# Performance work log

Hardware: AMD Instinct MI355X
Metric: run time of the kernel (lower is better)

## Reference

```python
import jax, jax.numpy as jnp
import numpy as np

B, S, H = 2, 1024, 4096
NQ, NKV, D = 32, 8, 128
I = 11008
EPS = 1e-5


def _rope_tables(seq_len, head_dim, base=10000.0):
    inv_freq = 1.0 / (base ** (np.arange(0, head_dim, 2, dtype=np.float32) / head_dim))
    t = np.arange(seq_len, dtype=np.float32)
    freqs = np.outer(t, inv_freq)                      # [S, D/2]
    emb = np.concatenate([freqs, freqs], axis=-1)      # [S, D]
    return jnp.asarray(np.cos(emb)), jnp.asarray(np.sin(emb))


def setup_inputs() -> dict:
    key = jax.random.key(0)
    ks = jax.random.split(key, 9)
    sc = 0.02
    cos, sin = _rope_tables(S, D)
    return {
        "x": jax.random.normal(ks[0], (B, S, H), jnp.float32),
        "cos": cos,
        "sin": sin,
        "attn_norm_w": jnp.ones((H,), jnp.float32),
        "ffn_norm_w": jnp.ones((H,), jnp.float32),
        "wq": jax.random.normal(ks[1], (H, NQ * D), jnp.float32) * sc,
        "wk": jax.random.normal(ks[2], (H, NKV * D), jnp.float32) * sc,
        "wv": jax.random.normal(ks[3], (H, NKV * D), jnp.float32) * sc,
        "wo": jax.random.normal(ks[4], (NQ * D, H), jnp.float32) * sc,
        "w_gate": jax.random.normal(ks[5], (H, I), jnp.float32) * sc,
        "w_up": jax.random.normal(ks[6], (H, I), jnp.float32) * sc,
        "w_down": jax.random.normal(ks[7], (I, H), jnp.float32) * sc,
    }


def _rmsnorm(x, w, eps=EPS):
    var = jnp.mean(jnp.square(x), axis=-1, keepdims=True)
    return x * jax.lax.rsqrt(var + eps) * w


def _rotate_half(x):
    x1, x2 = jnp.split(x, 2, axis=-1)
    return jnp.concatenate([-x2, x1], axis=-1)


def _apply_rope(q, k, cos, sin):
    # q: [B,S,NQ,D], k: [B,S,NKV,D]; cos/sin: [S,D] -> broadcast [1,S,1,D]
    c = cos[None, :, None, :]
    s = sin[None, :, None, :]
    return q * c + _rotate_half(q) * s, k * c + _rotate_half(k) * s


def reference(x, cos, sin, attn_norm_w, ffn_norm_w, wq, wk, wv, wo, w_gate, w_up, w_down):
    # ---- attention block (pre-norm, context/prefill path, causal) ----
    h_in = _rmsnorm(x, attn_norm_w)
    q = (h_in @ wq).reshape(B, S, NQ, D)
    k = (h_in @ wk).reshape(B, S, NKV, D)
    v = (h_in @ wv).reshape(B, S, NKV, D)
    q, k = _apply_rope(q, k, cos, sin)

    n_rep = NQ // NKV
    k = jnp.repeat(k, n_rep, axis=2)  # [B,S,NQ,D]
    v = jnp.repeat(v, n_rep, axis=2)

    scale = 1.0 / jnp.sqrt(jnp.float32(D))
    scores = jnp.einsum("bqhd,bkhd->bhqk", q, k) * scale  # [B,NQ,S,S]
    causal = jnp.tril(jnp.ones((S, S), bool))
    scores = jnp.where(causal[None, None], scores, -jnp.inf)
    probs = jax.nn.softmax(scores, axis=-1)
    attn = jnp.einsum("bhqk,bkhd->bqhd", probs, v).reshape(B, S, NQ * D)
    h = x + attn @ wo

    # ---- MLP block (pre-norm SwiGLU) ----
    m_in = _rmsnorm(h, ffn_norm_w)
    mlp = (jax.nn.silu(m_in @ w_gate) * (m_in @ w_up)) @ w_down
    return h + mlp
```

## Files before the change

### kernel.cpp

```cpp
#include <hip/hip_runtime.h>
#include <cstdint>
#include <cstddef>


typedef __bf16 bf16;
typedef __attribute__((ext_vector_type(8))) __bf16 bf16x8;
typedef __attribute__((ext_vector_type(4))) float f32x4;

#define GLDS16(gptr, lptr)                                                    \
  __builtin_amdgcn_global_load_lds(                                           \
      (const __attribute__((address_space(1))) void*)(gptr),                  \
      (__attribute__((address_space(3))) void*)(lptr), 16, 0, 0)

#define S_LEN 1024
#define H_DIM 4096
#define NQ_H 32
#define NKV_H 8
#define HD 128
#define I_DIM 11008

__global__ __launch_bounds__(256) void wtrans64_kernel(
    const float* __restrict__ src, bf16* __restrict__ dst, int K, int N,
    int tile_stride, int base) {
  const int tid = threadIdx.x;
  const int n0 = blockIdx.x * 64, k0 = blockIdx.y * 64;
  __shared__ float t[64][65];
  const int r = tid >> 4, c4 = (tid & 15) * 4;
#pragma unroll
  for (int j = 0; j < 4; j++) {
    const float4 v =
        *(const float4*)&src[(size_t)(k0 + r + j * 16) * N + n0 + c4];
    t[r + j * 16][c4 + 0] = v.x;
    t[r + j * 16][c4 + 1] = v.y;
    t[r + j * 16][c4 + 2] = v.z;
    t[r + j * 16][c4 + 3] = v.w;
  }
  __syncthreads();
  const int n = tid >> 2, kq = (tid & 3) * 16;
  bf16x8 o0, o1;
#pragma unroll
  for (int i = 0; i < 8; i++) {
    o0[i] = (bf16)t[kq + i][n];
    o1[i] = (bf16)t[kq + 8 + i][n];
  }
  const int ng = n0 + n;
  const size_t orow = (size_t)(ng >> 7) * tile_stride + (ng & 127) + base;
  *(bf16x8*)&dst[orow * K + k0 + kq] = o0;
  *(bf16x8*)&dst[orow * K + k0 + kq + 8] = o1;
}

__global__ __launch_bounds__(256) void rmsnorm_kernel(
    const float* __restrict__ x, const float* __restrict__ w,
    bf16* __restrict__ out) {
  const int row = blockIdx.x;
  const float4* xr = (const float4*)(x + (size_t)row * H_DIM);
  float4 v[4];
  float s = 0.f;
#pragma unroll
  for (int i = 0; i < 4; i++) {
    v[i] = xr[threadIdx.x + i * 256];
    s += v[i].x * v[i].x + v[i].y * v[i].y + v[i].z * v[i].z + v[i].w * v[i].w;
  }
#pragma unroll
  for (int m = 1; m < 64; m <<= 1) s += __shfl_xor(s, m);
  __shared__ float red[4];
  if ((threadIdx.x & 63) == 0) red[threadIdx.x >> 6] = s;
  __syncthreads();
  s = red[0] + red[1] + red[2] + red[3];
  const float r = rsqrtf(s * (1.f / H_DIM) + 1e-5f);
  bf16* o = out + (size_t)row * H_DIM;
  const float4* wr = (const float4*)w;
#pragma unroll
  for (int i = 0; i < 4; i++) {
    float4 wv = wr[threadIdx.x + i * 256];
    int idx = (threadIdx.x + i * 256) * 4;
    o[idx + 0] = (bf16)(v[i].x * r * wv.x);
    o[idx + 1] = (bf16)(v[i].y * r * wv.y);
    o[idx + 2] = (bf16)(v[i].z * r * wv.z);
    o[idx + 3] = (bf16)(v[i].w * r * wv.w);
  }
}

template <int BM, int MODE>
__global__ __launch_bounds__(512, 2) void gemm256(
    const bf16* __restrict__ A, const bf16* __restrict__ Bt,
    void* __restrict__ Cout, const float* __restrict__ resid, int N, int K,
    int mshift) {
  constexpr int MREP = BM / 32;
  constexpr int MQ = MREP / 2;
  constexpr int LA = BM / 128;
  constexpr int ABYTES = BM * 128;
  constexpr int BUFB = ABYTES + 32768;
  __shared__ __align__(16) char smem[2 * BUFB];

  const int tid = threadIdx.x;
  const int w = tid >> 6, lane = tid & 63;
  const int lr = lane & 15, quad = lane >> 4;
  const int wm = w & 1, wn = w >> 1;
  const int m0 = (blockIdx.x & ((1 << mshift) - 1)) * BM;
  const int n0 = (blockIdx.x >> mshift) * 256;
  const int NT = K >> 6;

  const int lrow = lane >> 3;
  const int lcbe = ((lane & 7) ^ lrow) << 3;
  const bf16* aS[2][LA];
#pragma unroll
  for (int h = 0; h < 2; h++)
#pragma unroll
    for (int j = 0; j < LA; j++)
      aS[h][j] =
          A + (size_t)(m0 + h * (BM / 2) + j * 64 + w * 8 + lrow) * K + lcbe;
  const bf16* bS[2][2];
#pragma unroll
  for (int h = 0; h < 2; h++)
#pragma unroll
    for (int j = 0; j < 2; j++)
      bS[h][j] =
          Bt + (size_t)(n0 + h * 128 + j * 64 + w * 8 + lrow) * K + lcbe;
  const int sdst = w * 1024;

#pragma unroll
  for (int h = 0; h < 2; h++)
#pragma unroll
    for (int j = 0; j < 2; j++)
      GLDS16(bS[h][j], smem + ABYTES + h * 16384 + j * 8192 + sdst);
#pragma unroll
  for (int h = 0; h < 2; h++)
#pragma unroll
    for (int j = 0; j < LA; j++)
      GLDS16(aS[h][j], smem + h * (BM * 64) + j * 8192 + sdst);
#pragma unroll
  for (int h = 0; h < 2; h++)
#pragma unroll
    for (int j = 0; j < 2; j++)
      GLDS16(bS[h][j] + 64, smem + BUFB + ABYTES + h * 16384 + j * 8192 + sdst);
  asm volatile("s_waitcnt vmcnt(4)" ::: "memory");
  __builtin_amdgcn_s_barrier();

  const int swz = (lr & 7) << 4;
  const int abase = (wm * (BM / 2) + lr) * 128;
  const int bbase = ABYTES + (wn * 64 + lr) * 128;
  const int pcb0 = (quad * 16) ^ swz;

  f32x4 acc[MREP][4] = {};
  bf16x8 af[MQ][2], bfr[2][2][2];

  for (int t = 0; t < NT; ++t) {
    char* cb_ = smem + (t & 1) * BUFB;
    char* nb_ = smem + ((t & 1) ^ 1) * BUFB;

#pragma unroll
    for (int i4 = 0; i4 < MQ; i4++)
#pragma unroll
      for (int kk = 0; kk < 2; kk++)
        af[i4][kk] = *(const bf16x8*)(cb_ + abase + i4 * (16 * 128) +
                                      (pcb0 ^ (kk * 64)));
#pragma unroll
    for (int j2 = 0; j2 < 2; j2++)
#pragma unroll
      for (int kk = 0; kk < 2; kk++)
        bfr[0][j2][kk] = *(const bf16x8*)(cb_ + bbase + j2 * (16 * 128) +
                                          (pcb0 ^ (kk * 64)));
    if (t + 1 < NT) {
#pragma unroll
      for (int j = 0; j < LA; j++)
        GLDS16(aS[0][j] + (size_t)(t + 1) * 64, nb_ + j * 8192 + sdst);
    }
    __builtin_amdgcn_s_barrier();
    asm volatile("s_waitcnt lgkmcnt(0)" ::: "memory");
    __builtin_amdgcn_sched_barrier(0);
    __builtin_amdgcn_s_setprio(1);
#pragma unroll
    for (int i4 = 0; i4 < MQ; i4++)
#pragma unroll
      for (int j2 = 0; j2 < 2; j2++)
#pragma unroll
        for (int kk = 0; kk < 2; kk++)
          acc[i4][j2] = __builtin_amdgcn_mfma_f32_16x16x32_bf16(
              af[i4][kk], bfr[0][j2][kk], acc[i4][j2], 0, 0, 0);
    __builtin_amdgcn_s_setprio(0);
    __builtin_amdgcn_s_barrier();

#pragma unroll
    for (int j2 = 0; j2 < 2; j2++)
#pragma unroll
      for (int kk = 0; kk < 2; kk++)
        bfr[1][j2][kk] =
            *(const bf16x8*)(cb_ + bbase + (32 + j2 * 16) * 128 +
                             (pcb0 ^ (kk * 64)));
    if (t + 1 < NT) {
#pragma unroll
      for (int j = 0; j < LA; j++)
        GLDS16(aS[1][j] + (size_t)(t + 1) * 64,
               nb_ + BM * 64 + j * 8192 + sdst);
    }
    __builtin_amdgcn_s_barrier();
    asm volatile("s_waitcnt lgkmcnt(0)" ::: "memory");
    __builtin_amdgcn_sched_barrier(0);
    __builtin_amdgcn_s_setprio(1);
#pragma unroll
    for (int i4 = 0; i4 < MQ; i4++)
#pragma unroll
      for (int j2 = 0; j2 < 2; j2++)
#pragma unroll
        for (int kk = 0; kk < 2; kk++)
          acc[i4][2 + j2] = __builtin_amdgcn_mfma_f32_16x16x32_bf16(
              af[i4][kk], bfr[1][j2][kk], acc[i4][2 + j2], 0, 0, 0);
    __builtin_amdgcn_s_setprio(0);
    __builtin_amdgcn_s_barrier();

#pragma unroll
    for (int i4 = 0; i4 < MQ; i4++)
#pragma unroll
      for (int kk = 0; kk < 2; kk++)
        af[i4][kk] =
            *(const bf16x8*)(cb_ + abase + ((BM / 4) + i4 * 16) * 128 +
                             (pcb0 ^ (kk * 64)));
    if (t + 2 < NT) {
#pragma unroll
      for (int j = 0; j < 2; j++)
        GLDS16(bS[0][j] + (size_t)(t + 2) * 64,
               cb_ + ABYTES + j * 8192 + sdst);
    }
    __builtin_amdgcn_s_barrier();
    asm volatile("s_waitcnt lgkmcnt(0)" ::: "memory");
    __builtin_amdgcn_sched_barrier(0);
    __builtin_amdgcn_s_setprio(1);
#pragma unroll
    for (int i4 = 0; i4 < MQ; i4++)
#pragma unroll
      for (int j2 = 0; j2 < 2; j2++)
#pragma unroll
        for (int kk = 0; kk < 2; kk++)
          acc[MQ + i4][j2] = __builtin_amdgcn_mfma_f32_16x16x32_bf16(
              af[i4][kk], bfr[0][j2][kk], acc[MQ + i4][j2], 0, 0, 0);
    __builtin_amdgcn_s_setprio(0);
    __builtin_amdgcn_s_barrier();

    if (t + 2 < NT) {
#pragma unroll
      for (int j = 0; j < 2; j++)
        GLDS16(bS[1][j] + (size_t)(t + 2) * 64,
               cb_ + ABYTES + 16384 + j * 8192 + sdst);
    }
    __builtin_amdgcn_s_barrier();
    asm volatile("s_waitcnt lgkmcnt(0)" ::: "memory");
    __builtin_amdgcn_sched_barrier(0);
    __builtin_amdgcn_s_setprio(1);
#pragma unroll
    for (int i4 = 0; i4 < MQ; i4++)
#pragma unroll
      for (int j2 = 0; j2 < 2; j2++)
#pragma unroll
        for (int kk = 0; kk < 2; kk++)
          acc[MQ + i4][2 + j2] = __builtin_amdgcn_mfma_f32_16x16x32_bf16(
              af[i4][kk], bfr[1][j2][kk], acc[MQ + i4][2 + j2], 0, 0, 0);
    __builtin_amdgcn_s_setprio(0);
    if (t + 2 < NT)
      asm volatile("s_waitcnt vmcnt(4)" ::: "memory");
    else
      asm volatile("s_waitcnt vmcnt(0)" ::: "memory");
    __builtin_amdgcn_s_barrier();
  }

#pragma unroll
  for (int ai = 0; ai < MREP; ai++)
#pragma unroll
    for (int bj = 0; bj < 4; bj++)
#pragma unroll
      for (int r = 0; r < 4; r++) {
        const size_t row = m0 + wm * (BM / 2) + ai * 16 + quad * 4 + r;
        const size_t col = n0 + wn * 64 + bj * 16 + lr;
        const float v = acc[ai][bj][r];
        if (MODE == 0)
          ((bf16*)Cout)[row * N + col] = (bf16)v;
        else
          ((float*)Cout)[row * N + col] = v + resid[row * N + col];
      }
}

__global__ __launch_bounds__(256) void rope_kernel(
    const bf16* __restrict__ qkv, const float* __restrict__ cosT,
    const float* __restrict__ sinT, bf16* __restrict__ qb,
    bf16* __restrict__ kb) {
  const int row = blockIdx.x;
  const int s = row & (S_LEN - 1);
  const bf16* base = qkv + (size_t)row * 6144;
  const float scale = 0.08838834764831845f;
  for (int p = threadIdx.x; p < 2560; p += 256) {
    const int hd = p >> 6;
    const int d = p & 63;
    const float c = cosT[s * HD + d], sn = sinT[s * HD + d];
    if (hd < NQ_H) {
      const bf16* qp = base + hd * HD;
      const float x1 = (float)qp[d], x2 = (float)qp[d + 64];
      bf16* o = qb + (size_t)row * H_DIM + hd * HD;
      o[d] = (bf16)((x1 * c - x2 * sn) * scale);
      o[d + 64] = (bf16)((x2 * c + x1 * sn) * scale);
    } else {
      const int kh = hd - NQ_H;
      const bf16* kp = base + H_DIM + kh * HD;
      const float x1 = (float)kp[d], x2 = (float)kp[d + 64];
      bf16* o = kb + (size_t)row * (NKV_H * HD) + kh * HD;
      o[d] = (bf16)(x1 * c - x2 * sn);
      o[d + 64] = (bf16)(x2 * c + x1 * sn);
    }
  }
}

__global__ __launch_bounds__(256) void vtrans_kernel(
    const bf16* __restrict__ qkv, bf16* __restrict__ vt) {
  const int tx = threadIdx.x & 31, ty = threadIdx.x >> 5;
  const int s0 = blockIdx.x * 32, d0 = blockIdx.y * 32;
  const int b = blockIdx.z >> 3, kv = blockIdx.z & 7;
  __shared__ float t[32][33];
#pragma unroll
  for (int j = 0; j < 4; j++) {
    const int s = s0 + ty + j * 8;
    t[ty + j * 8][tx] =
        (float)qkv[(size_t)(b * S_LEN + s) * 6144 + 5120 + kv * HD + d0 + tx];
  }
  __syncthreads();
#pragma unroll
  for (int j = 0; j < 4; j++) {
    const int d = d0 + ty + j * 8;
    vt[((size_t)(b * NKV_H + kv) * HD + d) * S_LEN + s0 + tx] =
        (bf16)t[tx][ty + j * 8];
  }
}

__global__ __launch_bounds__(256) void attn_fwd(
    const bf16* __restrict__ Qb, const bf16* __restrict__ Kb,
    const bf16* __restrict__ Vtb, bf16* __restrict__ Ob) {
  __shared__ __align__(16) bf16 Ks[16 * 512];
  __shared__ __align__(16) bf16 Vs[16 * 512];
  __shared__ __align__(16) bf16 Ps[16 * 512];
  const int tid = threadIdx.x;
  const int wave = tid >> 6, lane = tid & 63;
  const int lr = lane & 15, quad = lane >> 4;
  const int qt = blockIdx.x, h = blockIdx.y, b = blockIdx.z;
  const int kv = h >> 2;
  const int qrow0 = qt * 128 + wave * 32;

  bf16x8 qf[2][4];
#pragma unroll
  for (int mi = 0; mi < 2; mi++)
#pragma unroll
    for (int ks = 0; ks < 4; ks++)
      qf[mi][ks] = *(const bf16x8*)&Qb[(size_t)(b * S_LEN + qrow0 + mi * 16 + lr) *
                                           H_DIM +
                                       h * HD + ks * 32 + quad * 8];

  f32x4 oacc[2][8] = {};
  float m_i[2][4], l_i[2][4];
#pragma unroll
  for (int mi = 0; mi < 2; mi++)
#pragma unroll
    for (int r = 0; r < 4; r++) {
      m_i[mi][r] = -__builtin_inff();
      l_i[mi][r] = 0.f;
    }

  const int nk = 2 * (qt + 1);
  const int maxrow = qrow0 + 31;
  const int srow = lane >> 2;
  const int scol = (lane & 3) * 8;

  for (int kt = 0; kt < nk; kt++) {
    const int k0 = kt * 64;
    __syncthreads();
#pragma unroll
    for (int i = 0; i < 4; i++) {
      const int c = wave * 4 + i;
      {
        const int ks = c >> 2, sc = c & 3;
        const int key = sc * 16 + srow;
        GLDS16(Kb + (size_t)(b * S_LEN + k0 + key) * (NKV_H * HD) + kv * HD +
                   ks * 32 + scol,
               Ks + c * 512);
      }
      {
        const int ks2 = c >> 3, sc2 = c & 7;
        const int d = sc2 * 16 + srow;
        GLDS16(Vtb + ((size_t)(b * NKV_H + kv) * HD + d) * S_LEN + k0 +
                   ks2 * 32 + scol,
               Vs + c * 512);
      }
    }
    __syncthreads();
    const bool active = (k0 <= maxrow);
    float alpha[2][4];
    if (active) {
      f32x4 sacc[2][4];
#pragma unroll
      for (int mi = 0; mi < 2; mi++)
#pragma unroll
        for (int nj = 0; nj < 4; nj++) sacc[mi][nj] = (f32x4){0.f, 0.f, 0.f, 0.f};
#pragma unroll
      for (int ks = 0; ks < 4; ks++) {
        bf16x8 kf[4];
#pragma unroll
        for (int nj = 0; nj < 4; nj++)
          kf[nj] = *(const bf16x8*)&Ks[ks * 2048 + (nj * 16 + lr) * 32 + quad * 8];
#pragma unroll
        for (int mi = 0; mi < 2; mi++)
#pragma unroll
          for (int nj = 0; nj < 4; nj++)
            sacc[mi][nj] = __builtin_amdgcn_mfma_f32_16x16x32_bf16(
                qf[mi][ks], kf[nj], sacc[mi][nj], 0, 0, 0);
      }
#pragma unroll
      for (int mi = 0; mi < 2; mi++) {
#pragma unroll
        for (int r = 0; r < 4; r++) {
          const int row = qrow0 + mi * 16 + quad * 4 + r;
          float best = -__builtin_inff();
#pragma unroll
          for (int nj = 0; nj < 4; nj++) {
            const int col = k0 + nj * 16 + lr;
            if (col > row) sacc[mi][nj][r] = -__builtin_inff();
            best = fmaxf(best, sacc[mi][nj][r]);
          }
#pragma unroll
          for (int m = 1; m < 16; m <<= 1)
            best = fmaxf(best, __shfl_xor(best, m));
          const float mnew = fmaxf(m_i[mi][r], best);
          alpha[mi][r] = __expf(m_i[mi][r] - mnew);
          m_i[mi][r] = mnew;
          float ssum = 0.f;
#pragma unroll
          for (int nj = 0; nj < 4; nj++) {
            const float p = __expf(sacc[mi][nj][r] - mnew);
            sacc[mi][nj][r] = p;
            ssum += p;
          }
#pragma unroll
          for (int m = 1; m < 16; m <<= 1) ssum += __shfl_xor(ssum, m);
          l_i[mi][r] = l_i[mi][r] * alpha[mi][r] + ssum;
        }
      }
#pragma unroll
      for (int mi = 0; mi < 2; mi++)
#pragma unroll
        for (int dj = 0; dj < 8; dj++)
#pragma unroll
          for (int r = 0; r < 4; r++) oacc[mi][dj][r] *= alpha[mi][r];
#pragma unroll
      for (int mi = 0; mi < 2; mi++)
#pragma unroll
        for (int nj = 0; nj < 4; nj++) {
          const int ks2 = nj >> 1;
          const int k32 = (nj & 1) * 16 + lr;
#pragma unroll
          for (int r = 0; r < 4; r++) {
            const int rowl = wave * 32 + mi * 16 + quad * 4 + r;
            Ps[ks2 * 4096 + rowl * 32 + k32] = (bf16)sacc[mi][nj][r];
          }
        }
    }
    __syncthreads();
    if (active) {
#pragma unroll
      for (int ks2 = 0; ks2 < 2; ks2++) {
        bf16x8 pf[2], vf[8];
#pragma unroll
        for (int mi = 0; mi < 2; mi++)
          pf[mi] = *(const bf16x8*)&Ps[ks2 * 4096 +
                                       (wave * 32 + mi * 16 + lr) * 32 + quad * 8];
#pragma unroll
        for (int dj = 0; dj < 8; dj++)
          vf[dj] = *(const bf16x8*)&Vs[ks2 * 4096 + (dj * 16 + lr) * 32 + quad * 8];
#pragma unroll
        for (int mi = 0; mi < 2; mi++)
#pragma unroll
          for (int dj = 0; dj < 8; dj++)
            oacc[mi][dj] = __builtin_amdgcn_mfma_f32_16x16x32_bf16(
                pf[mi], vf[dj], oacc[mi][dj], 0, 0, 0);
      }
    }
  }
#pragma unroll
  for (int mi = 0; mi < 2; mi++)
#pragma unroll
    for (int r = 0; r < 4; r++) {
      const float rinv = 1.f / l_i[mi][r];
      const size_t row = (size_t)b * S_LEN + qrow0 + mi * 16 + quad * 4 + r;
#pragma unroll
      for (int dj = 0; dj < 8; dj++)
        Ob[row * H_DIM + h * HD + dj * 16 + lr] =
            (bf16)(oacc[mi][dj][r] * rinv);
    }
}

__global__ __launch_bounds__(256) void swiglu_kernel(
    const bf16* __restrict__ gu, bf16* __restrict__ act) {
  const int gid = blockIdx.x * 256 + threadIdx.x;
  const int row = gid / 1376;
  const int c8 = (gid % 1376) * 8;
  const size_t gbase = (size_t)row * 22016 + (size_t)(c8 >> 7) * 256 + (c8 & 127);
  bf16x8 g = *(const bf16x8*)&gu[gbase];
  bf16x8 u = *(const bf16x8*)&gu[gbase + 128];
  bf16x8 o;
#pragma unroll
  for (int j = 0; j < 8; j++) {
    const float gf = (float)g[j];
    const float sg = gf / (1.f + __expf(-gf));
    o[j] = (bf16)(sg * (float)u[j]);
  }
  *(bf16x8*)&act[(size_t)row * I_DIM + c8] = o;
}

extern "C" void kernel_launch(void* const* d_in, const int* in_sizes, int n_in,
                              void* d_out, int out_size, void* d_ws,
                              size_t ws_size, hipStream_t stream) {
  const float* x = (const float*)d_in[0];
  const float* cosT = (const float*)d_in[1];
  const float* sinT = (const float*)d_in[2];
  const float* anw = (const float*)d_in[3];
  const float* fnw = (const float*)d_in[4];
  const float* wq = (const float*)d_in[5];
  const float* wk = (const float*)d_in[6];
  const float* wv = (const float*)d_in[7];
  const float* wo = (const float*)d_in[8];
  const float* wg = (const float*)d_in[9];
  const float* wu = (const float*)d_in[10];
  const float* wd = (const float*)d_in[11];

  char* ws = (char*)d_ws;
  size_t off = 0;
  auto alloc = [&](size_t bytes) -> void* {
    void* p = ws + off;
    off += (bytes + 255) & ~(size_t)255;
    return p;
  };
  const size_t M = 2048;
  bf16* WGUt = (bf16*)alloc(22016ULL * 4096 * 2);
  bf16* WDt = (bf16*)alloc(4096ULL * I_DIM * 2);
  char* R1 = (char*)alloc(90177536);
  char* bufY = (char*)alloc(83886080);
  float* H2 = (float*)alloc(M * 4096 * 4);
  bf16* MINb = (bf16*)alloc(M * 4096 * 2);

  bf16* WQKVt = (bf16*)R1;
  bf16* WOt = (bf16*)(R1 + 50331648);
  bf16* GU = (bf16*)R1;
  bf16* HIN = (bf16*)bufY;
  bf16* QKVb = HIN + M * 4096;
  bf16* QB = QKVb + M * 6144;
  bf16* KB = QB + M * 4096;
  bf16* VT = KB + M * 1024;
  bf16* ATTN = VT + M * 1024;
  bf16* ACT = (bf16*)bufY;

  wtrans64_kernel<<<dim3(64, 64), 256, 0, stream>>>(wq, WQKVt, 4096, 4096, 128, 0);
  wtrans64_kernel<<<dim3(16, 64), 256, 0, stream>>>(wk, WQKVt + 4096ULL * 4096, 4096, 1024, 128, 0);
  wtrans64_kernel<<<dim3(16, 64), 256, 0, stream>>>(wv, WQKVt + 5120ULL * 4096, 4096, 1024, 128, 0);
  wtrans64_kernel<<<dim3(64, 64), 256, 0, stream>>>(wo, WOt, 4096, 4096, 128, 0);
  wtrans64_kernel<<<dim3(172, 64), 256, 0, stream>>>(wg, WGUt, 4096, I_DIM, 256, 0);
  wtrans64_kernel<<<dim3(172, 64), 256, 0, stream>>>(wu, WGUt, 4096, I_DIM, 256, 128);
  wtrans64_kernel<<<dim3(64, 172), 256, 0, stream>>>(wd, WDt, I_DIM, 4096, 128, 0);

  rmsnorm_kernel<<<2048, 256, 0, stream>>>(x, anw, HIN);
  gemm256<256, 0><<<8 * 24, 512, 0, stream>>>(HIN, WQKVt, QKVb, nullptr, 6144, 4096, 3);
  rope_kernel<<<2048, 256, 0, stream>>>(QKVb, cosT, sinT, QB, KB);
  vtrans_kernel<<<dim3(32, 4, 16), 256, 0, stream>>>(QKVb, VT);
  attn_fwd<<<dim3(8, 32, 2), 256, 0, stream>>>(QB, KB, VT, ATTN);
  gemm256<128, 2><<<16 * 16, 512, 0, stream>>>(ATTN, WOt, H2, x, 4096, 4096, 4);
  rmsnorm_kernel<<<2048, 256, 0, stream>>>(H2, fnw, MINb);
  gemm256<256, 0><<<8 * 86, 512, 0, stream>>>(MINb, WGUt, GU, nullptr, 22016, 4096, 3);
  swiglu_kernel<<<11008, 256, 0, stream>>>(GU, ACT);
  gemm256<128, 2><<<16 * 16, 512, 0, stream>>>(ACT, WDt, d_out, H2, 4096, 11008, 4);
}
```

Before: 1.546 ms.

## Restructure GEMM inner loop to split K halves and prefetch fragments across phases

Reorganizes the 4-phase MFMA loop so each phase processes one K-half (kk) of all four B column fragments instead of one column half for both K-halves. LDS fragment loads for the next phase are issued before the current MFMAs, and partial lgkmcnt waits replace full drains, so LDS reads overlap with matrix math. It also remaps the block index across 8 groups, intended to improve L2 locality or XCD distribution. Barrier placement and vmcnt thresholds change, which risks races or stalls if the counts are wrong.

```diff
diff --git a/kernel.cpp b/kernel.cpp
--- a/kernel.cpp
+++ b/kernel.cpp
@@ -18,6 +18,18 @@
 #define NKV_H 8
 #define HD 128
 #define I_DIM 11008
+
+template <int N>
+__device__ __forceinline__ void waitl() {
+  asm volatile("s_waitcnt lgkmcnt(%0)" ::"n"(N) : "memory");
+}
+template <int N>
+__device__ __forceinline__ void waitv() {
+  asm volatile("s_waitcnt vmcnt(%0)" ::"n"(N) : "memory");
+}
+__device__ __forceinline__ void barr() {
+  asm volatile("s_barrier" ::: "memory");
+}
 
 __global__ __launch_bounds__(256) void wtrans64_kernel(
     const float* __restrict__ src, bf16* __restrict__ dst, int K, int N,
@@ -97,8 +109,9 @@
   const int w = tid >> 6, lane = tid & 63;
   const int lr = lane & 15, quad = lane >> 4;
   const int wm = w & 1, wn = w >> 1;
-  const int m0 = (blockIdx.x & ((1 << mshift) - 1)) * BM;
-  const int n0 = (blockIdx.x >> mshift) * 256;
+  const int bid = (blockIdx.x & 7) * ((int)gridDim.x >> 3) + (blockIdx.x >> 3);
+  const int m0 = (bid & ((1 << mshift) - 1)) * BM;
+  const int n0 = (bid >> mshift) * 256;
   const int NT = K >> 6;
 
   const int lrow = lane >> 3;
@@ -134,8 +147,8 @@
 #pragma unroll
     for (int j = 0; j < 2; j++)
       GLDS16(bS[h][j] + 64, smem + BUFB + ABYTES + h * 16384 + j * 8192 + sdst);
-  asm volatile("s_waitcnt vmcnt(4)" ::: "memory");
-  __builtin_amdgcn_s_barrier();
+  waitv<4>();
+  barr();
 
   const int swz = (lr & 7) << 4;
   const int abase = (wm * (BM / 2) + lr) * 128;
@@ -143,124 +156,111 @@
   const int pcb0 = (quad * 16) ^ swz;
 
   f32x4 acc[MREP][4] = {};
-  bf16x8 af[MQ][2], bfr[2][2][2];
+  bf16x8 afA[MQ], afB[MQ], bK0[4], bK1[4];
+
+#pragma unroll
+  for (int i = 0; i < MQ; i++)
+    afA[i] = *(const bf16x8*)(smem + abase + i * 2048 + pcb0);
+#pragma unroll
+  for (int j = 0; j < 4; j++)
+    bK0[j] = *(const bf16x8*)(smem + bbase + j * 2048 + pcb0);
 
   for (int t = 0; t < NT; ++t) {
     char* cb_ = smem + (t & 1) * BUFB;
     char* nb_ = smem + ((t & 1) ^ 1) * BUFB;
 
-#pragma unroll
-    for (int i4 = 0; i4 < MQ; i4++)
-#pragma unroll
-      for (int kk = 0; kk < 2; kk++)
-        af[i4][kk] = *(const bf16x8*)(cb_ + abase + i4 * (16 * 128) +
-                                      (pcb0 ^ (kk * 64)));
-#pragma unroll
-    for (int j2 = 0; j2 < 2; j2++)
-#pragma unroll
-      for (int kk = 0; kk < 2; kk++)
-        bfr[0][j2][kk] = *(const bf16x8*)(cb_ + bbase + j2 * (16 * 128) +
-                                          (pcb0 ^ (kk * 64)));
+    barr();
+#pragma unroll
+    for (int i = 0; i < MQ; i++)
+      afB[i] = *(const bf16x8*)(cb_ + abase + i * 2048 + (pcb0 ^ 64));
+#pragma unroll
+    for (int j = 0; j < 4; j++)
+      bK1[j] = *(const bf16x8*)(cb_ + bbase + j * 2048 + (pcb0 ^ 64));
     if (t + 1 < NT) {
 #pragma unroll
       for (int j = 0; j < LA; j++)
         GLDS16(aS[0][j] + (size_t)(t + 1) * 64, nb_ + j * 8192 + sdst);
     }
-    __builtin_amdgcn_s_barrier();
-    asm volatile("s_waitcnt lgkmcnt(0)" ::: "memory");
+    waitl<MQ + 4>();
     __builtin_amdgcn_sched_barrier(0);
     __builtin_amdgcn_s_setprio(1);
 #pragma unroll
-    for (int i4 = 0; i4 < MQ; i4++)
-#pragma unroll
-      for (int j2 = 0; j2 < 2; j2++)
-#pragma unroll
-        for (int kk = 0; kk < 2; kk++)
-          acc[i4][j2] = __builtin_amdgcn_mfma_f32_16x16x32_bf16(
-              af[i4][kk], bfr[0][j2][kk], acc[i4][j2], 0, 0, 0);
+    for (int i = 0; i < MQ; i++)
+#pragma unroll
+      for (int j = 0; j < 4; j++)
+        acc[i][j] = __builtin_amdgcn_mfma_f32_16x16x32_bf16(afA[i], bK0[j],
+                                                            acc[i][j], 0, 0, 0);
     __builtin_amdgcn_s_setprio(0);
-    __builtin_amdgcn_s_barrier();
-
-#pragma unroll
-    for (int j2 = 0; j2 < 2; j2++)
-#pragma unroll
-      for (int kk = 0; kk < 2; kk++)
-        bfr[1][j2][kk] =
-            *(const bf16x8*)(cb_ + bbase + (32 + j2 * 16) * 128 +
-                             (pcb0 ^ (kk * 64)));
+
+    barr();
+#pragma unroll
+    for (int i = 0; i < MQ; i++)
+      afA[i] = *(const bf16x8*)(cb_ + abase + (BM / 4 + i * 16) * 128 + pcb0);
     if (t + 1 < NT) {
 #pragma unroll
       for (int j = 0; j < LA; j++)
         GLDS16(aS[1][j] + (size_t)(t + 1) * 64,
                nb_ + BM * 64 + j * 8192 + sdst);
     }
-    __builtin_amdgcn_s_barrier();
-    asm volatile("s_waitcnt lgkmcnt(0)" ::: "memory");
+    waitl<MQ>();
     __builtin_amdgcn_sched_barrier(0);
     __builtin_amdgcn_s_setprio(1);
 #pragma unroll
-    for (int i4 = 0; i4 < MQ; i4++)
-#pragma unroll
-      for (int j2 = 0; j2 < 2; j2++)
-#pragma unroll
-        for (int kk = 0; kk < 2; kk++)
-          acc[i4][2 + j2] = __builtin_amdgcn_mfma_f32_16x16x32_bf16(
-              af[i4][kk], bfr[1][j2][kk], acc[i4][2 + j2], 0, 0, 0);
+    for (int i = 0; i < MQ; i++)
+#pragma unroll
+      for (int j = 0; j < 4; j++)
+        acc[i][j] = __builtin_amdgcn_mfma_f32_16x16x32_bf16(afB[i], bK1[j],
+                                                            acc[i][j], 0, 0, 0);
     __builtin_amdgcn_s_setprio(0);
-    __builtin_amdgcn_s_barrier();
-
-#pragma unroll
-    for (int i4 = 0; i4 < MQ; i4++)
-#pragma unroll
-      for (int kk = 0; kk < 2; kk++)
-        af[i4][kk] =
-            *(const bf16x8*)(cb_ + abase + ((BM / 4) + i4 * 16) * 128 +
-                             (pcb0 ^ (kk * 64)));
+
+    barr();
+#pragma unroll
+    for (int i = 0; i < MQ; i++)
+      afB[i] =
+          *(const bf16x8*)(cb_ + abase + (BM / 4 + i * 16) * 128 + (pcb0 ^ 64));
     if (t + 2 < NT) {
 #pragma unroll
       for (int j = 0; j < 2; j++)
-        GLDS16(bS[0][j] + (size_t)(t + 2) * 64,
-               cb_ + ABYTES + j * 8192 + sdst);
-    }
-    __builtin_amdgcn_s_barrier();
-    asm volatile("s_waitcnt lgkmcnt(0)" ::: "memory");
+        GLDS16(bS[0][j] + (size_t)(t + 2) * 64, cb_ + ABYTES + j * 8192 + sdst);
+    }
+    waitl<MQ>();
     __builtin_amdgcn_sched_barrier(0);
     __builtin_amdgcn_s_setprio(1);
 #pragma unroll
-    for (int i4 = 0; i4 < MQ; i4++)
-#pragma unroll
-      for (int j2 = 0; j2 < 2; j2++)
-#pragma unroll
-        for (int kk = 0; kk < 2; kk++)
-          acc[MQ + i4][j2] = __builtin_amdgcn_mfma_f32_16x16x32_bf16(
-              af[i4][kk], bfr[0][j2][kk], acc[MQ + i4][j2], 0, 0, 0);
+    for (int i = 0; i < MQ; i++)
+#pragma unroll
+      for (int j = 0; j < 4; j++)
+        acc[MQ + i][j] = __builtin_amdgcn_mfma_f32_16x16x32_bf16(
+            afA[i], bK0[j], acc[MQ + i][j], 0, 0, 0);
     __builtin_amdgcn_s_setprio(0);
-    __builtin_amdgcn_s_barrier();
-
+
+    if (t + 2 < NT)
+      waitv<2>();
+    else
+      waitv<0>();
+    barr();
+#pragma unroll
+    for (int i = 0; i < MQ; i++)
+      afA[i] = *(const bf16x8*)(nb_ + abase + i * 2048 + pcb0);
+#pragma unroll
+    for (int j = 0; j < 4; j++)
+      bK0[j] = *(const bf16x8*)(nb_ + bbase + j * 2048 + pcb0);
     if (t + 2 < NT) {
 #pragma unroll
       for (int j = 0; j < 2; j++)
         GLDS16(bS[1][j] + (size_t)(t + 2) * 64,
                cb_ + ABYTES + 16384 + j * 8192 + sdst);
     }
-    __builtin_amdgcn_s_barrier();
-    asm volatile("s_waitcnt lgkmcnt(0)" ::: "memory");
+    waitl<MQ + 4>();
     __builtin_amdgcn_sched_barrier(0);
     __builtin_amdgcn_s_setprio(1);
 #pragma unroll
-    for (int i4 = 0; i4 < MQ; i4++)
-#pragma unroll
-      for (int j2 = 0; j2 < 2; j2++)
-#pragma unroll
-        for (int kk = 0; kk < 2; kk++)
-          acc[MQ + i4][2 + j2] = __builtin_amdgcn_mfma_f32_16x16x32_bf16(
-              af[i4][kk], bfr[1][j2][kk], acc[MQ + i4][2 + j2], 0, 0, 0);
+    for (int i = 0; i < MQ; i++)
+#pragma unroll
+      for (int j = 0; j < 4; j++)
+        acc[MQ + i][j] = __builtin_amdgcn_mfma_f32_16x16x32_bf16(
+            afB[i], bK1[j], acc[MQ + i][j], 0, 0, 0);
     __builtin_amdgcn_s_setprio(0);
-    if (t + 2 < NT)
-      asm volatile("s_waitcnt vmcnt(4)" ::: "memory");
-    else
-      asm volatile("s_waitcnt vmcnt(0)" ::: "memory");
-    __builtin_amdgcn_s_barrier();
   }
 
 #pragma unroll
```

Result: faster. 1.509 ms (-2.4%).
